# Kernel optimization log

Measured on AMD Instinct MI355X. Metric: run time of the kernel, lower is better.

Reference implementation:

```python
import jax, jax.numpy as jnp
import numpy as np

N_A = 100000; N_B = 100000; E = 1600000
H = 128; OUT = 16; G = 256; D_A = 64; D_B = 32


def setup_inputs() -> dict:
    key = jax.random.key(0)
    ks = jax.random.split(key, 24)
    f32 = jnp.float32
    def w(k, shape, fan_in):
        return jax.random.normal(k, shape, dtype=f32) / np.sqrt(fan_in)
    inp = {
        'x_a': jax.random.normal(ks[0], (N_A, D_A), dtype=f32),
        'x_b': jax.random.normal(ks[1], (N_B, D_B), dtype=f32),
        'ei_ab': jax.random.randint(ks[2], (2, E), 0, N_A),  # row0: src in a, row1: dst in b
        'ei_ba': jax.random.randint(ks[3], (2, E), 0, N_B),
        'ei_aa': jax.random.randint(ks[4], (2, E), 0, N_A),
        'batch_a': jnp.sort(jax.random.randint(ks[5], (N_A,), 0, G)),
        'batch_b': jnp.sort(jax.random.randint(ks[6], (N_B,), 0, G)),
        # node-type input embeddings
        'Wemb_a': w(ks[7], (D_A, H), D_A), 'bemb_a': jnp.zeros((H,), f32),
        'Wemb_b': w(ks[8], (D_B, H), D_B), 'bemb_b': jnp.zeros((H,), f32),
        # SAGEConv params per relation: lin_l (with bias) on aggregated, lin_r (no bias) on root
        'Wl_ab': w(ks[9], (H, H), H), 'bl_ab': jnp.zeros((H,), f32), 'Wr_ab': w(ks[10], (H, H), H),
        'Wl_ba': w(ks[11], (H, H), H), 'bl_ba': jnp.zeros((H,), f32), 'Wr_ba': w(ks[12], (H, H), H),
        'Wl_aa': w(ks[13], (H, H), H), 'bl_aa': jnp.zeros((H,), f32), 'Wr_aa': w(ks[14], (H, H), H),
        # output head
        'Wout': w(ks[15], (H, OUT), H), 'bout': jnp.zeros((OUT,), f32),
    }
    return inp


def _sage(x_src, x_dst, ei, Wl, bl, Wr, n_dst):
    # mean aggregation of source features over incoming edges, then transform + root
    msg = x_src[ei[0]]                                        # [E, H] gather
    s = jax.ops.segment_sum(msg, ei[1], num_segments=n_dst)   # [n_dst, H]
    cnt = jax.ops.segment_sum(jnp.ones((ei.shape[1], 1), x_src.dtype), ei[1], num_segments=n_dst)
    agg = s / jnp.maximum(cnt, 1.0)
    return agg @ Wl + bl + x_dst @ Wr


def _mean_pool(x, batch, num_graphs):
    s = jax.ops.segment_sum(x, batch, num_segments=num_graphs)
    cnt = jax.ops.segment_sum(jnp.ones((x.shape[0], 1), x.dtype), batch, num_segments=num_graphs)
    return s / jnp.maximum(cnt, 1.0)


def reference(x_a, x_b, ei_ab, ei_ba, ei_aa, batch_a, batch_b,
              Wemb_a, bemb_a, Wemb_b, bemb_b,
              Wl_ab, bl_ab, Wr_ab, Wl_ba, bl_ba, Wr_ba, Wl_aa, bl_aa, Wr_aa,
              Wout, bout):
    # per-type input projection
    h_a = x_a @ Wemb_a + bemb_a            # [N_A, H]
    h_b = x_b @ Wemb_b + bemb_b            # [N_B, H]
    # HeteroConv: one SAGEConv per relation, mean over relations per dst type
    m_b = _sage(h_a, h_b, ei_ab, Wl_ab, bl_ab, Wr_ab, N_B)          # dst 'b': 1 relation
    m_a1 = _sage(h_b, h_a, ei_ba, Wl_ba, bl_ba, Wr_ba, N_A)
    m_a2 = _sage(h_a, h_a, ei_aa, Wl_aa, bl_aa, Wr_aa, N_A)
    h_a2 = 0.5 * (m_a1 + m_a2)                                      # dst 'a': mean of 2 relations
    h_b2 = m_b
    # ReLU + per-type global mean pool + mean over node types
    p_a = _mean_pool(jax.nn.relu(h_a2), batch_a, G)                 # [G, H]
    p_b = _mean_pool(jax.nn.relu(h_b2), batch_b, G)
    x = 0.5 * (p_a + p_b)
    return x @ Wout + bout                                          # [G, OUT]
```

## Files before the change

kernel.cpp:

```cpp
#include <hip/hip_runtime.h>

#define NA 100000
#define NB 100000
#define NEDGE 1600000
#define HD 128
#define OUTD 16
#define NG 256
#define DA 64
#define DB 32

#define BIN_SHIFT 9
#define BIN_W 512
#define NBINS_R 196
#define NBINS 588
#define PADBIN 10240
#define EPB 8192
#define ECHUNKS 196

typedef unsigned int uint_t;
typedef unsigned short ushort_t;
typedef unsigned char uchar_t;
typedef __bf16 bf16_t;
typedef bf16_t bf16x8 __attribute__((ext_vector_type(8)));
typedef float f32x4 __attribute__((ext_vector_type(4)));
typedef float f32x2 __attribute__((ext_vector_type(2)));

__device__ __forceinline__ float bflo(uint_t u) {
    union { uint_t i; float f; } c; c.i = u << 16; return c.f;
}
__device__ __forceinline__ float bfhi(uint_t u) {
    union { uint_t i; float f; } c; c.i = u & 0xffff0000u; return c.f;
}
__device__ __forceinline__ float bf2f(ushort_t u) {
    union { uint_t i; float f; } c; c.i = ((uint_t)u) << 16; return c.f;
}
__device__ __forceinline__ uint_t f2bf(float f) {
    union { float f; uint_t i; } c; c.f = f;
    uint_t r = c.i + 0x7FFFu + ((c.i >> 16) & 1u);
    return r >> 16;
}
__device__ __forceinline__ uint_t pack2bf(float lo, float hi) {
    return f2bf(lo) | (f2bf(hi) << 16);
}

__global__ void __launch_bounds__(256)
prep_misc_kernel(const float* __restrict__ Wl_ab, const float* __restrict__ Wr_ab,
                 const float* __restrict__ Wl_ba, const float* __restrict__ Wl_aa,
                 const float* __restrict__ Wr_ba, const float* __restrict__ Wr_aa,
                 const float* __restrict__ Wemb_a, const float* __restrict__ Wemb_b,
                 ushort_t* __restrict__ wt_fb, ushort_t* __restrict__ wt_pa,
                 ushort_t* __restrict__ wt_ea, ushort_t* __restrict__ wt_eb,
                 const float* __restrict__ bl_ba, const float* __restrict__ bl_aa,
                 float* __restrict__ bias_pa,
                 const int* __restrict__ batch_a, const int* __restrict__ batch_b,
                 float* __restrict__ ga, float* __restrict__ gb)
{
    const int bx = blockIdx.x;
    __align__(16) ushort_t tmp[8];
    if (bx >= 40) {
        if (bx <= 43) {
            const int id = (bx - 40) * 256 + threadIdx.x;
            const int kk = id >> 9, ni = (id >> 6) & 7, l = id & 63;
            const int col = ni * 16 + (l & 15);
            const int k0 = kk * 32 + (l >> 4) * 8;
#pragma unroll
            for (int j = 0; j < 8; ++j) tmp[j] = (ushort_t)f2bf(Wemb_a[(k0 + j) * HD + col]);
            *reinterpret_cast<uint4*>(wt_ea + (size_t)id * 8) = *reinterpret_cast<const uint4*>(tmp);
            return;
        }
        if (bx <= 45) {
            const int id = (bx - 44) * 256 + threadIdx.x;
            const int ni = id >> 6, l = id & 63;
            const int col = ni * 16 + (l & 15);
            const int k0 = (l >> 4) * 8;
#pragma unroll
            for (int j = 0; j < 8; ++j) tmp[j] = (ushort_t)f2bf(Wemb_b[(k0 + j) * HD + col]);
            *reinterpret_cast<uint4*>(wt_eb + (size_t)id * 8) = *reinterpret_cast<const uint4*>(tmp);
            return;
        }
        if (bx == 46) {
            if (threadIdx.x < HD) bias_pa[threadIdx.x] = bl_ba[threadIdx.x] + bl_aa[threadIdx.x];
            return;
        }
        const int g = threadIdx.x;
        const int* batch = (bx == 48) ? batch_b : batch_a;
        float* outp = (bx == 48) ? gb : ga;
        const int n = NA;
        int lo0 = 0, hi0 = n;
        while (lo0 < hi0) { const int mid = (lo0 + hi0) >> 1; if (batch[mid] < g) lo0 = mid + 1; else hi0 = mid; }
        int lo1 = 0, hi1 = n;
        while (lo1 < hi1) { const int mid = (lo1 + hi1) >> 1; if (batch[mid] < g + 1) lo1 = mid + 1; else hi1 = mid; }
        outp[g] = (float)(lo1 - lo0);
        return;
    }
    const int m = bx >> 3;
    const int id = (bx & 7) * 256 + threadIdx.x;
    const int kk = id >> 9, ni = (id >> 6) & 7, l = id & 63;
    const int col = ni * 16 + (l & 15);
    const int k0 = kk * 32 + (l >> 4) * 8;
    const float* src = (m == 0) ? Wl_ab : (m == 1) ? Wr_ab : (m == 2) ? Wl_ba
                     : (m == 3) ? Wl_aa : Wr_ba;
#pragma unroll
    for (int j = 0; j < 8; ++j) {
        float v = src[(k0 + j) * HD + col];
        if (m == 4) v += Wr_aa[(k0 + j) * HD + col];
        tmp[j] = (ushort_t)f2bf(v);
    }
    const int half = ni >> 2, nih = ni & 3;
    const size_t eoff = (size_t)half * 8192 + ((kk * 4 + nih) * 64 + l) * 8;
    ushort_t* dst = (m < 2) ? (wt_fb + (size_t)m * 16384) : (wt_pa + (size_t)(m - 2) * 16384);
    *reinterpret_cast<uint4*>(dst + eoff) = *reinterpret_cast<const uint4*>(tmp);
}

template<int K>
__global__ void __launch_bounds__(256)
emb_mfma(const float* __restrict__ x, const ushort_t* __restrict__ wtf,
         const float* __restrict__ bias, ushort_t* __restrict__ h, int n)
{
    constexpr int KST = K / 32;
    __shared__ ushort_t wlds[K * HD];
    for (int i = threadIdx.x * 8; i < K * HD; i += 2048)
        *reinterpret_cast<uint4*>(wlds + i) = *reinterpret_cast<const uint4*>(wtf + i);
    __syncthreads();

    const int l = threadIdx.x & 63, w = threadIdx.x >> 6;
    const int lo = l & 15, hi = l >> 4;
    const int row_base = blockIdx.x * 128 + w * 32;

    f32x4 acc[2][8];
    const f32x4 zero = {0.f, 0.f, 0.f, 0.f};
#pragma unroll
    for (int mi = 0; mi < 2; ++mi)
#pragma unroll
        for (int ni = 0; ni < 8; ++ni) acc[mi][ni] = zero;

    bf16x8 a[2][KST];
#pragma unroll
    for (int mi = 0; mi < 2; ++mi) {
        int r = row_base + mi * 16 + lo;
        r = min(r, n - 1);
        const float* xr = x + (size_t)r * K + hi * 8;
#pragma unroll
        for (int kk = 0; kk < KST; ++kk) {
            const float4 f0 = *reinterpret_cast<const float4*>(xr + kk * 32);
            const float4 f1 = *reinterpret_cast<const float4*>(xr + kk * 32 + 4);
            __align__(16) ushort_t us[8];
            us[0] = (ushort_t)f2bf(f0.x); us[1] = (ushort_t)f2bf(f0.y);
            us[2] = (ushort_t)f2bf(f0.z); us[3] = (ushort_t)f2bf(f0.w);
            us[4] = (ushort_t)f2bf(f1.x); us[5] = (ushort_t)f2bf(f1.y);
            us[6] = (ushort_t)f2bf(f1.z); us[7] = (ushort_t)f2bf(f1.w);
            a[mi][kk] = *reinterpret_cast<const bf16x8*>(us);
        }
    }
#pragma unroll
    for (int kk = 0; kk < KST; ++kk) {
#pragma unroll
        for (int ni = 0; ni < 8; ++ni) {
            const bf16x8 b = *reinterpret_cast<const bf16x8*>(wlds + ((kk * 8 + ni) * 64 + l) * 8);
            acc[0][ni] = __builtin_amdgcn_mfma_f32_16x16x32_bf16(a[0][kk], b, acc[0][ni], 0, 0, 0);
            acc[1][ni] = __builtin_amdgcn_mfma_f32_16x16x32_bf16(a[1][kk], b, acc[1][ni], 0, 0, 0);
        }
    }
#pragma unroll
    for (int ni = 0; ni < 8; ++ni) {
        const int col = ni * 16 + lo;
        const float bv = bias[col];
#pragma unroll
        for (int mi = 0; mi < 2; ++mi) {
            const f32x4 v = acc[mi][ni];
#pragma unroll
            for (int r = 0; r < 4; ++r) {
                const int row = row_base + mi * 16 + hi * 4 + r;
                if (row < n) h[(size_t)row * HD + col] = (ushort_t)f2bf(v[r] + bv);
            }
        }
    }
}

__global__ void __launch_bounds__(256)
conv8_kernel(const ushort_t* __restrict__ h, uchar_t* __restrict__ h8, long n8)
{
    for (long i = (long)blockIdx.x * 256 + threadIdx.x; i < n8; i += (long)gridDim.x * 256) {
        const uint4 v = *reinterpret_cast<const uint4*>(h + i * 8);
        uint_t lo = (uint_t)__builtin_amdgcn_cvt_pk_fp8_f32(bflo(v.x), bfhi(v.x), 0, false);
        lo = (uint_t)__builtin_amdgcn_cvt_pk_fp8_f32(bflo(v.y), bfhi(v.y), lo, true);
        uint_t hi = (uint_t)__builtin_amdgcn_cvt_pk_fp8_f32(bflo(v.z), bfhi(v.z), 0, false);
        hi = (uint_t)__builtin_amdgcn_cvt_pk_fp8_f32(bflo(v.w), bfhi(v.w), hi, true);
        uint2 o; o.x = lo; o.y = hi;
        *reinterpret_cast<uint2*>(h8 + i * 8) = o;
    }
}

__global__ void __launch_bounds__(256)
part3_kernel(const int* __restrict__ ei_ab, const int* __restrict__ ei_ba,
             const int* __restrict__ ei_aa, int* __restrict__ bincnt,
             uint_t* __restrict__ binned)
{
    __shared__ uint_t sorted[EPB];
    __shared__ int lh[NBINS_R];
    __shared__ int lbase[NBINS_R];
    __shared__ int gbase[NBINS_R];
    __shared__ int lcur[NBINS_R];
    __shared__ int sc[256];
    const int r = blockIdx.y;
    const int* ei = (r == 0) ? ei_ab : (r == 1) ? ei_ba : ei_aa;
    const int t = threadIdx.x;
    for (int i = t; i < NBINS_R; i += 256) lh[i] = 0;
    __syncthreads();
    const int e0 = blockIdx.x * EPB;
    const int e1 = min(e0 + EPB, NEDGE);
    for (int e = e0 + t; e < e1; e += 256)
        atomicAdd(&lh[ei[NEDGE + e] >> BIN_SHIFT], 1);
    __syncthreads();
    {
        const int v = (t < NBINS_R) ? lh[t] : 0;
        sc[t] = v; __syncthreads();
        for (int d = 1; d < 256; d <<= 1) {
            const int x = (t >= d) ? sc[t - d] : 0;
            __syncthreads();
            sc[t] += x;
            __syncthreads();
        }
        if (t < NBINS_R) {
            const int ex = sc[t] - v;
            lbase[t] = ex; lcur[t] = ex;
            gbase[t] = v ? atomicAdd(&bincnt[r * NBINS_R + t], v) : 0;
        }
    }
    __syncthreads();
    for (int e = e0 + t; e < e1; e += 256) {
        const int dst = ei[NEDGE + e];
        const int src = ei[e];
        const int bin = dst >> BIN_SHIFT;
        const int pos = atomicAdd(&lcur[bin], 1);
        sorted[pos] = ((uint_t)(dst & (BIN_W - 1)) << 17) | (uint_t)src;
    }
    __syncthreads();
    const int wid = t >> 6, lane = t & 63;
    for (int b = wid; b < NBINS_R; b += 4) {
        const int cnt = lh[b], lb = lbase[b];
        uint_t* dst = binned + (size_t)(r * NBINS_R + b) * PADBIN + gbase[b];
        for (int k = lane; k < cnt; k += 64) dst[k] = sorted[lb + k];
    }
}

__global__ void __launch_bounds__(256)
binfill3_kernel(const uint_t* __restrict__ binned, const int* __restrict__ bincnt,
                int* __restrict__ off3, int* __restrict__ cnt3, int* __restrict__ csr3)
{
    __shared__ int hist[BIN_W];
    __shared__ int A[BIN_W];
    __shared__ int cursor[BIN_W];
    const int b = blockIdx.x;
    const int r = blockIdx.y;
    const int g = r * NBINS_R + b;
    const int start = g * PADBIN;
    const int end = start + bincnt[g];
    const int t = threadIdx.x;
    const int i0 = t, i1 = t + 256;
    hist[i0] = 0; hist[i1] = 0;
    __syncthreads();
    for (int j = start + t; j < end; j += 256)
        atomicAdd(&hist[binned[j] >> 17], 1);
    __syncthreads();
    A[i0] = hist[i0]; A[i1] = hist[i1];
    __syncthreads();
    for (int d = 1; d < BIN_W; d <<= 1) {
        const int x0 = (i0 >= d) ? A[i0 - d] : 0;
        const int x1 = (i1 >= d) ? A[i1 - d] : 0;
        __syncthreads();
        A[i0] += x0; A[i1] += x1;
        __syncthreads();
    }
    const int node0 = b * BIN_W;
#pragma unroll
    for (int q = 0; q < 2; ++q) {
        const int i = t + q * 256;
        const int ex = start + A[i] - hist[i];
        cursor[i] = ex;
        const int node = node0 + i;
        if (node < NA) { off3[r * NA + node] = ex; cnt3[r * NA + node] = hist[i]; }
    }
    __syncthreads();
    for (int j = start + t; j < end; j += 256) {
        const uint_t p = binned[j];
        const int pos = atomicAdd(&cursor[p >> 17], 1);
        csr3[pos] = (int)(p & 0x1FFFFu);
    }
}

__global__ void __launch_bounds__(256)
gather3_kernel(const uchar_t* __restrict__ h8_a, const uchar_t* __restrict__ h8_b,
               const int* __restrict__ csr3, const int* __restrict__ off3,
               const int* __restrict__ cnt3,
               ushort_t* __restrict__ s_ab, ushort_t* __restrict__ s_ba,
               ushort_t* __restrict__ s_aa)
{
    const int r = blockIdx.y;
    const uchar_t* hsrc = (r == 1) ? h8_b : h8_a;
    ushort_t* s = (r == 0) ? s_ab : (r == 1) ? s_ba : s_aa;
    const int* off = off3 + r * NA;
    const int* cnt = cnt3 + r * NA;
    const int wid = threadIdx.x >> 6, lane = threadIdx.x & 63;
    const int hl = lane & 31;
    const int nw = gridDim.x * 4;
    for (int node = blockIdx.x * 4 + wid; node < NA; node += nw) {
        const int o0 = off[node], deg = cnt[node];
        const int o1 = o0 + deg;
        float ax0 = 0.f, ax1 = 0.f, ax2 = 0.f, ax3 = 0.f;
        int j = o0;
        for (; j + 8 <= o1; j += 8) {
            const int s0 = csr3[j],     s1 = csr3[j + 1], s2 = csr3[j + 2], s3 = csr3[j + 3];
            const int s4 = csr3[j + 4], s5 = csr3[j + 5], s6 = csr3[j + 6], s7 = csr3[j + 7];
            const int sA = (lane & 32) ? s1 : s0;
            const int sB = (lane & 32) ? s3 : s2;
            const int sC = (lane & 32) ? s5 : s4;
            const int sD = (lane & 32) ? s7 : s6;
            const uint_t vA = *reinterpret_cast<const uint_t*>(hsrc + (size_t)sA * HD + hl * 4);
            const uint_t vB = *reinterpret_cast<const uint_t*>(hsrc + (size_t)sB * HD + hl * 4);
            const uint_t vC = *reinterpret_cast<const uint_t*>(hsrc + (size_t)sC * HD + hl * 4);
            const uint_t vD = *reinterpret_cast<const uint_t*>(hsrc + (size_t)sD * HD + hl * 4);
            const f32x2 a0 = __builtin_amdgcn_cvt_pk_f32_fp8(vA, false), a1 = __builtin_amdgcn_cvt_pk_f32_fp8(vA, true);
            const f32x2 b0 = __builtin_amdgcn_cvt_pk_f32_fp8(vB, false), b1 = __builtin_amdgcn_cvt_pk_f32_fp8(vB, true);
            const f32x2 c0 = __builtin_amdgcn_cvt_pk_f32_fp8(vC, false), c1 = __builtin_amdgcn_cvt_pk_f32_fp8(vC, true);
            const f32x2 d0 = __builtin_amdgcn_cvt_pk_f32_fp8(vD, false), d1 = __builtin_amdgcn_cvt_pk_f32_fp8(vD, true);
            ax0 += (a0[0] + b0[0]) + (c0[0] + d0[0]);
            ax1 += (a0[1] + b0[1]) + (c0[1] + d0[1]);
            ax2 += (a1[0] + b1[0]) + (c1[0] + d1[0]);
            ax3 += (a1[1] + b1[1]) + (c1[1] + d1[1]);
        }
        for (; j + 2 <= o1; j += 2) {
            const int s0 = csr3[j], s1 = csr3[j + 1];
            const int sA = (lane & 32) ? s1 : s0;
            const uint_t vA = *reinterpret_cast<const uint_t*>(hsrc + (size_t)sA * HD + hl * 4);
            const f32x2 a0 = __builtin_amdgcn_cvt_pk_f32_fp8(vA, false), a1 = __builtin_amdgcn_cvt_pk_f32_fp8(vA, true);
            ax0 += a0[0]; ax1 += a0[1]; ax2 += a1[0]; ax3 += a1[1];
        }
        if (j < o1) {
            const int s0 = csr3[j];
            const uint_t vA = *reinterpret_cast<const uint_t*>(hsrc + (size_t)s0 * HD + hl * 4);
            if (!(lane & 32)) {
                const f32x2 a0 = __builtin_amdgcn_cvt_pk_f32_fp8(vA, false), a1 = __builtin_amdgcn_cvt_pk_f32_fp8(vA, true);
                ax0 += a0[0]; ax1 += a0[1]; ax2 += a1[0]; ax3 += a1[1];
            }
        }
        ax0 += __shfl_xor(ax0, 32); ax1 += __shfl_xor(ax1, 32);
        ax2 += __shfl_xor(ax2, 32); ax3 += __shfl_xor(ax3, 32);
        if (!(lane & 32)) {
            const float inv = 1.0f / fmaxf((float)deg, 1.0f);
            uint2 wv;
            wv.x = pack2bf(ax0 * inv, ax1 * inv);
            wv.y = pack2bf(ax2 * inv, ax3 * inv);
            *reinterpret_cast<uint2*>(s + (size_t)node * HD + hl * 4) = wv;
        }
    }
}

template<int NSRC, int SCALE_HALF>
__global__ void __launch_bounds__(256, 4)
mfma_task(const ushort_t* __restrict__ x0, const ushort_t* __restrict__ x1,
          const ushort_t* __restrict__ x2,
          const ushort_t* __restrict__ wtf, const float* __restrict__ bias,
          ushort_t* __restrict__ m_out, int n)
{
    extern __shared__ char smem[];
    ushort_t* wlds = (ushort_t*)smem;
    const int half = blockIdx.y;
    for (int i = threadIdx.x * 8; i < NSRC * 8192; i += 2048) {
        const int s = i >> 13, off = i & 8191;
        *reinterpret_cast<uint4*>(wlds + i) =
            *reinterpret_cast<const uint4*>(wtf + (size_t)s * 16384 + half * 8192 + off);
    }
    __syncthreads();

    const int l  = threadIdx.x & 63, w = threadIdx.x >> 6;
    const int lo = l & 15, hi = l >> 4;
    const int row_base = blockIdx.x * 128 + w * 32;

    f32x4 acc[2][4];
    const f32x4 zero = {0.f, 0.f, 0.f, 0.f};
#pragma unroll
    for (int mi = 0; mi < 2; ++mi)
#pragma unroll
        for (int ni = 0; ni < 4; ++ni) acc[mi][ni] = zero;

#pragma unroll
    for (int s = 0; s < NSRC; ++s) {
        const ushort_t* xs = (s == 0) ? x0 : (s == 1) ? x1 : x2;
        bf16x8 a[2][4];
#pragma unroll
        for (int mi = 0; mi < 2; ++mi) {
            int r = row_base + mi * 16 + lo;
            r = min(r, n - 1);
            const ushort_t* xr = xs + (size_t)r * HD + hi * 8;
#pragma unroll
            for (int kk = 0; kk < 4; ++kk)
                a[mi][kk] = *reinterpret_cast<const bf16x8*>(xr + kk * 32);
        }
        const ushort_t* wm = wlds + s * 8192;
#pragma unroll
        for (int kk = 0; kk < 4; ++kk) {
#pragma unroll
            for (int nih = 0; nih < 4; ++nih) {
                const bf16x8 b = *reinterpret_cast<const bf16x8*>(wm + ((kk * 4 + nih) * 64 + l) * 8);
                acc[0][nih] = __builtin_amdgcn_mfma_f32_16x16x32_bf16(a[0][kk], b, acc[0][nih], 0, 0, 0);
                acc[1][nih] = __builtin_amdgcn_mfma_f32_16x16x32_bf16(a[1][kk], b, acc[1][nih], 0, 0, 0);
            }
        }
    }

#pragma unroll
    for (int nih = 0; nih < 4; ++nih) {
        const int col = half * 64 + nih * 16 + lo;
        const float bv = bias[col];
#pragma unroll
        for (int mi = 0; mi < 2; ++mi) {
            const f32x4 v = acc[mi][nih];
#pragma unroll
            for (int r = 0; r < 4; ++r) {
                const int row = row_base + mi * 16 + hi * 4 + r;
                if (row < n) {
                    float val = v[r] + bv;
                    if (SCALE_HALF) val *= 0.5f;
                    m_out[(size_t)row * HD + col] = (ushort_t)f2bf(fmaxf(val, 0.f));
                }
            }
        }
    }
}

__global__ void __launch_bounds__(256)
pool_kernel(const ushort_t* __restrict__ m_a, const ushort_t* __restrict__ m_b,
            const int* __restrict__ batch_a, const int* __restrict__ batch_b,
            float* __restrict__ pool_a, float* __restrict__ pool_b)
{
    const ushort_t* m = blockIdx.y ? m_b : m_a;
    const int* batch = blockIdx.y ? batch_b : batch_a;
    float* pool = blockIdx.y ? pool_b : pool_a;
    const int col = threadIdx.x & 127;
    const int rh = threadIdx.x >> 7;
    int row = blockIdx.x * 256 + rh * 128;
    const int rend = min(row + 128, NA);
    if (row >= rend) return;
    float acc = 0.f;
    int gcur = batch[row];
    for (; row < rend; ++row) {
        const int g = batch[row];
        if (g != gcur) {
            unsafeAtomicAdd(pool + (size_t)gcur * HD + col, acc);
            acc = 0.f; gcur = g;
        }
        acc += bf2f(m[(size_t)row * HD + col]);
    }
    unsafeAtomicAdd(pool + (size_t)gcur * HD + col, acc);
}

__global__ void final_kernel(const float* __restrict__ pa, const float* __restrict__ pb,
                             const float* __restrict__ ga, const float* __restrict__ gb,
                             const float* __restrict__ Wout, const float* __restrict__ bout,
                             float* __restrict__ out)
{
    const int g = blockIdx.x;
    const int lane = threadIdx.x;
    const float inva = 1.0f / fmaxf(ga[g], 1.0f);
    const float invb = 1.0f / fmaxf(gb[g], 1.0f);
    if (lane < OUTD) {
        float acc = bout[lane];
        for (int k = 0; k < HD; ++k) {
            const float x = 0.5f * (pa[g * HD + k] * inva + pb[g * HD + k] * invb);
            acc = fmaf(x, Wout[k * OUTD + lane], acc);
        }
        out[g * OUTD + lane] = acc;
    }
}

extern "C" void kernel_launch(void* const* d_in, const int* in_sizes, int n_in,
                              void* d_out, int out_size, void* d_ws, size_t ws_size,
                              hipStream_t stream)
{
    const float* x_a     = (const float*)d_in[0];
    const float* x_b     = (const float*)d_in[1];
    const int*   ei_ab   = (const int*)d_in[2];
    const int*   ei_ba   = (const int*)d_in[3];
    const int*   ei_aa   = (const int*)d_in[4];
    const int*   batch_a = (const int*)d_in[5];
    const int*   batch_b = (const int*)d_in[6];
    const float* Wemb_a  = (const float*)d_in[7];
    const float* bemb_a  = (const float*)d_in[8];
    const float* Wemb_b  = (const float*)d_in[9];
    const float* bemb_b  = (const float*)d_in[10];
    const float* Wl_ab   = (const float*)d_in[11];
    const float* bl_ab   = (const float*)d_in[12];
    const float* Wr_ab   = (const float*)d_in[13];
    const float* Wl_ba   = (const float*)d_in[14];
    const float* bl_ba   = (const float*)d_in[15];
    const float* Wr_ba   = (const float*)d_in[16];
    const float* Wl_aa   = (const float*)d_in[17];
    const float* bl_aa   = (const float*)d_in[18];
    const float* Wr_aa   = (const float*)d_in[19];
    const float* Wout    = (const float*)d_in[20];
    const float* bout    = (const float*)d_in[21];
    float* out = (float*)d_out;

    char* p = (char*)d_ws;
    ushort_t* h_a  = (ushort_t*)p; p += (size_t)NA * HD * 2;
    ushort_t* h_b  = (ushort_t*)p; p += (size_t)NB * HD * 2;
    ushort_t* s_ab = (ushort_t*)p; p += (size_t)NB * HD * 2;
    ushort_t* s_ba = (ushort_t*)p; p += (size_t)NA * HD * 2;
    ushort_t* s_aa = (ushort_t*)p; p += (size_t)NA * HD * 2;
    ushort_t* m_a  = (ushort_t*)p; p += (size_t)NA * HD * 2;
    ushort_t* m_b  = (ushort_t*)p; p += (size_t)NB * HD * 2;
    uchar_t* h8_a  = (uchar_t*)p;  p += (size_t)NA * HD;
    uchar_t* h8_b  = (uchar_t*)p;  p += (size_t)NB * HD;
    int* csr3   = (int*)p;  p += (size_t)NBINS * PADBIN * 4;
    uint_t* binned = (uint_t*)p; p += (size_t)NBINS * PADBIN * 4;
    int* off3   = (int*)p;  p += (size_t)3 * NA * 4;
    int* cnt3   = (int*)p;  p += (size_t)3 * NA * 4;
    int* bincnt = (int*)p;  p += (NBINS + 4) * 4;
    float* pool_a = (float*)p; p += (size_t)NG * HD * 4;
    float* pool_b = (float*)p; p += (size_t)NG * HD * 4;
    float* gcnt_a = (float*)p; p += NG * 4;
    float* gcnt_b = (float*)p; p += NG * 4;
    ushort_t* wt_fb = (ushort_t*)p; p += 2 * 16384 * 2;
    ushort_t* wt_pa = (ushort_t*)p; p += 3 * 16384 * 2;
    ushort_t* wt_ea = (ushort_t*)p; p += 64 * HD * 2;
    ushort_t* wt_eb = (ushort_t*)p; p += 32 * HD * 2;
    float* bias_pa  = (float*)p;    p += HD * 4;

    const int GT = (NA + 127) / 128;

    hipMemsetAsync(pool_a, 0, (size_t)2 * NG * HD * 4, stream);
    hipMemsetAsync(bincnt, 0, (size_t)NBINS * 4, stream);

    prep_misc_kernel<<<49, 256, 0, stream>>>(Wl_ab, Wr_ab, Wl_ba, Wl_aa, Wr_ba, Wr_aa,
                                             Wemb_a, Wemb_b, wt_fb, wt_pa, wt_ea, wt_eb,
                                             bl_ba, bl_aa, bias_pa,
                                             batch_a, batch_b, gcnt_a, gcnt_b);

    emb_mfma<DA><<<GT, 256, 0, stream>>>(x_a, wt_ea, bemb_a, h_a, NA);
    emb_mfma<DB><<<GT, 256, 0, stream>>>(x_b, wt_eb, bemb_b, h_b, NB);
    conv8_kernel<<<2048, 256, 0, stream>>>(h_a, h8_a, (long)(NA + NB) * HD / 8);

    part3_kernel<<<dim3(ECHUNKS, 3), 256, 0, stream>>>(ei_ab, ei_ba, ei_aa, bincnt, binned);
    binfill3_kernel<<<dim3(NBINS_R, 3), 256, 0, stream>>>(binned, bincnt, off3, cnt3, csr3);

    gather3_kernel<<<dim3(2048, 3), 256, 0, stream>>>(h8_a, h8_b, csr3, off3, cnt3, s_ab, s_ba, s_aa);

    const int lds_b = 2 * 16384;
    const int lds_a = 3 * 16384;
    hipFuncSetAttribute((const void*)mfma_task<2, 0>, hipFuncAttributeMaxDynamicSharedMemorySize, lds_b);
    hipFuncSetAttribute((const void*)mfma_task<3, 1>, hipFuncAttributeMaxDynamicSharedMemorySize, lds_a);

    mfma_task<2, 0><<<dim3(GT, 2), 256, lds_b, stream>>>(s_ab, h_b, nullptr, wt_fb, bl_ab, m_b, NB);
    mfma_task<3, 1><<<dim3(GT, 2), 256, lds_a, stream>>>(s_ba, s_aa, h_a, wt_pa, bias_pa, m_a, NA);

    pool_kernel<<<dim3((NA + 255) / 256, 2), 256, 0, stream>>>(m_a, m_b, batch_a, batch_b, pool_a, pool_b);

    final_kernel<<<NG, 64, 0, stream>>>(pool_a, pool_b, gcnt_a, gcnt_b, Wout, bout, out);
}
```

Measured before the change: 454.6 us.

## Fuse embedding with fp8 conversion, merge MFMA launches, deepen gather unroll

The two embedding kernels are merged into one launch, and each now writes the fp8 copy directly, which removes the separate conversion pass over h. The gather loop is unrolled to 16 edges per iteration with packed f32x2 accumulation so more loads are in flight. The two SAGE MFMA kernels are merged into one launch with a reordered tile/half mapping, and the pool kernel uses smaller row chunks for more blocks. The trade-off is more atomics in pooling, more register pressure in the gather loop, and fp8 bytes written through scattered per-element stores.

New measurement: 399.7 us. -12.1%, faster.

```diff
diff --git a/kernel.cpp b/kernel.cpp
--- a/kernel.cpp
+++ b/kernel.cpp
@@ -41,6 +41,9 @@
 }
 __device__ __forceinline__ uint_t pack2bf(float lo, float hi) {
     return f2bf(lo) | (f2bf(hi) << 16);
+}
+__device__ __forceinline__ uchar_t f2fp8(float v) {
+    return (uchar_t)(__builtin_amdgcn_cvt_pk_fp8_f32(v, v, 0, false) & 0xff);
 }
 
 __global__ void __launch_bounds__(256)
@@ -113,12 +116,12 @@
 }
 
 template<int K>
-__global__ void __launch_bounds__(256)
-emb_mfma(const float* __restrict__ x, const ushort_t* __restrict__ wtf,
-         const float* __restrict__ bias, ushort_t* __restrict__ h, int n)
+__device__ __forceinline__ void
+emb_body(const float* __restrict__ x, const ushort_t* __restrict__ wtf,
+         const float* __restrict__ bias, ushort_t* __restrict__ h,
+         uchar_t* __restrict__ h8, int n, ushort_t* wlds)
 {
     constexpr int KST = K / 32;
-    __shared__ ushort_t wlds[K * HD];
     for (int i = threadIdx.x * 8; i < K * HD; i += 2048)
         *reinterpret_cast<uint4*>(wlds + i) = *reinterpret_cast<const uint4*>(wtf + i);
     __syncthreads();
@@ -171,24 +174,26 @@
 #pragma unroll
             for (int r = 0; r < 4; ++r) {
                 const int row = row_base + mi * 16 + hi * 4 + r;
-                if (row < n) h[(size_t)row * HD + col] = (ushort_t)f2bf(v[r] + bv);
-            }
-        }
-    }
-}
-
-__global__ void __launch_bounds__(256)
-conv8_kernel(const ushort_t* __restrict__ h, uchar_t* __restrict__ h8, long n8)
-{
-    for (long i = (long)blockIdx.x * 256 + threadIdx.x; i < n8; i += (long)gridDim.x * 256) {
-        const uint4 v = *reinterpret_cast<const uint4*>(h + i * 8);
-        uint_t lo = (uint_t)__builtin_amdgcn_cvt_pk_fp8_f32(bflo(v.x), bfhi(v.x), 0, false);
-        lo = (uint_t)__builtin_amdgcn_cvt_pk_fp8_f32(bflo(v.y), bfhi(v.y), lo, true);
-        uint_t hi = (uint_t)__builtin_amdgcn_cvt_pk_fp8_f32(bflo(v.z), bfhi(v.z), 0, false);
-        hi = (uint_t)__builtin_amdgcn_cvt_pk_fp8_f32(bflo(v.w), bfhi(v.w), hi, true);
-        uint2 o; o.x = lo; o.y = hi;
-        *reinterpret_cast<uint2*>(h8 + i * 8) = o;
-    }
+                if (row < n) {
+                    const float val = v[r] + bv;
+                    h[(size_t)row * HD + col] = (ushort_t)f2bf(val);
+                    h8[(size_t)row * HD + col] = f2fp8(val);
+                }
+            }
+        }
+    }
+}
+
+__global__ void __launch_bounds__(256)
+emb2_kernel(const float* __restrict__ x_a, const float* __restrict__ x_b,
+            const ushort_t* __restrict__ wt_ea, const ushort_t* __restrict__ wt_eb,
+            const float* __restrict__ bemb_a, const float* __restrict__ bemb_b,
+            ushort_t* __restrict__ h_a, ushort_t* __restrict__ h_b,
+            uchar_t* __restrict__ h8_a, uchar_t* __restrict__ h8_b)
+{
+    __shared__ ushort_t wlds[DA * HD];
+    if (blockIdx.y == 0) emb_body<DA>(x_a, wt_ea, bemb_a, h_a, h8_a, NA, wlds);
+    else                 emb_body<DB>(x_b, wt_eb, bemb_b, h_b, h8_b, NB, wlds);
 }
 
 __global__ void __launch_bounds__(256)
@@ -303,50 +308,57 @@
     const int* cnt = cnt3 + r * NA;
     const int wid = threadIdx.x >> 6, lane = threadIdx.x & 63;
     const int hl = lane & 31;
+    const int sel = (lane >> 5) & 1;
     const int nw = gridDim.x * 4;
     for (int node = blockIdx.x * 4 + wid; node < NA; node += nw) {
         const int o0 = off[node], deg = cnt[node];
         const int o1 = o0 + deg;
-        float ax0 = 0.f, ax1 = 0.f, ax2 = 0.f, ax3 = 0.f;
+        f32x2 acc01 = {0.f, 0.f}, acc23 = {0.f, 0.f};
         int j = o0;
-        for (; j + 8 <= o1; j += 8) {
-            const int s0 = csr3[j],     s1 = csr3[j + 1], s2 = csr3[j + 2], s3 = csr3[j + 3];
-            const int s4 = csr3[j + 4], s5 = csr3[j + 5], s6 = csr3[j + 6], s7 = csr3[j + 7];
-            const int sA = (lane & 32) ? s1 : s0;
-            const int sB = (lane & 32) ? s3 : s2;
-            const int sC = (lane & 32) ? s5 : s4;
-            const int sD = (lane & 32) ? s7 : s6;
-            const uint_t vA = *reinterpret_cast<const uint_t*>(hsrc + (size_t)sA * HD + hl * 4);
-            const uint_t vB = *reinterpret_cast<const uint_t*>(hsrc + (size_t)sB * HD + hl * 4);
-            const uint_t vC = *reinterpret_cast<const uint_t*>(hsrc + (size_t)sC * HD + hl * 4);
-            const uint_t vD = *reinterpret_cast<const uint_t*>(hsrc + (size_t)sD * HD + hl * 4);
-            const f32x2 a0 = __builtin_amdgcn_cvt_pk_f32_fp8(vA, false), a1 = __builtin_amdgcn_cvt_pk_f32_fp8(vA, true);
-            const f32x2 b0 = __builtin_amdgcn_cvt_pk_f32_fp8(vB, false), b1 = __builtin_amdgcn_cvt_pk_f32_fp8(vB, true);
-            const f32x2 c0 = __builtin_amdgcn_cvt_pk_f32_fp8(vC, false), c1 = __builtin_amdgcn_cvt_pk_f32_fp8(vC, true);
-            const f32x2 d0 = __builtin_amdgcn_cvt_pk_f32_fp8(vD, false), d1 = __builtin_amdgcn_cvt_pk_f32_fp8(vD, true);
-            ax0 += (a0[0] + b0[0]) + (c0[0] + d0[0]);
-            ax1 += (a0[1] + b0[1]) + (c0[1] + d0[1]);
-            ax2 += (a1[0] + b1[0]) + (c1[0] + d1[0]);
-            ax3 += (a1[1] + b1[1]) + (c1[1] + d1[1]);
+        for (; j + 16 <= o1; j += 16) {
+            uint_t vv[8];
+#pragma unroll
+            for (int q = 0; q < 8; ++q) {
+                const int sE = csr3[j + 2 * q + sel];
+                vv[q] = *reinterpret_cast<const uint_t*>(hsrc + (size_t)sE * HD + hl * 4);
+            }
+#pragma unroll
+            for (int q = 0; q < 8; ++q) {
+                acc01 += __builtin_amdgcn_cvt_pk_f32_fp8(vv[q], false);
+                acc23 += __builtin_amdgcn_cvt_pk_f32_fp8(vv[q], true);
+            }
+        }
+        for (; j + 4 <= o1; j += 4) {
+            uint_t vv[2];
+#pragma unroll
+            for (int q = 0; q < 2; ++q) {
+                const int sE = csr3[j + 2 * q + sel];
+                vv[q] = *reinterpret_cast<const uint_t*>(hsrc + (size_t)sE * HD + hl * 4);
+            }
+#pragma unroll
+            for (int q = 0; q < 2; ++q) {
+                acc01 += __builtin_amdgcn_cvt_pk_f32_fp8(vv[q], false);
+                acc23 += __builtin_amdgcn_cvt_pk_f32_fp8(vv[q], true);
+            }
         }
         for (; j + 2 <= o1; j += 2) {
-            const int s0 = csr3[j], s1 = csr3[j + 1];
-            const int sA = (lane & 32) ? s1 : s0;
-            const uint_t vA = *reinterpret_cast<const uint_t*>(hsrc + (size_t)sA * HD + hl * 4);
-            const f32x2 a0 = __builtin_amdgcn_cvt_pk_f32_fp8(vA, false), a1 = __builtin_amdgcn_cvt_pk_f32_fp8(vA, true);
-            ax0 += a0[0]; ax1 += a0[1]; ax2 += a1[0]; ax3 += a1[1];
+            const int sE = csr3[j + sel];
+            const uint_t v = *reinterpret_cast<const uint_t*>(hsrc + (size_t)sE * HD + hl * 4);
+            acc01 += __builtin_amdgcn_cvt_pk_f32_fp8(v, false);
+            acc23 += __builtin_amdgcn_cvt_pk_f32_fp8(v, true);
         }
         if (j < o1) {
-            const int s0 = csr3[j];
-            const uint_t vA = *reinterpret_cast<const uint_t*>(hsrc + (size_t)s0 * HD + hl * 4);
-            if (!(lane & 32)) {
-                const f32x2 a0 = __builtin_amdgcn_cvt_pk_f32_fp8(vA, false), a1 = __builtin_amdgcn_cvt_pk_f32_fp8(vA, true);
-                ax0 += a0[0]; ax1 += a0[1]; ax2 += a1[0]; ax3 += a1[1];
-            }
-        }
+            const int sE = csr3[min(j + sel, o1 - 1)];
+            const uint_t v = *reinterpret_cast<const uint_t*>(hsrc + (size_t)sE * HD + hl * 4);
+            if (!sel) {
+                acc01 += __builtin_amdgcn_cvt_pk_f32_fp8(v, false);
+                acc23 += __builtin_amdgcn_cvt_pk_f32_fp8(v, true);
+            }
+        }
+        float ax0 = acc01[0], ax1 = acc01[1], ax2 = acc23[0], ax3 = acc23[1];
         ax0 += __shfl_xor(ax0, 32); ax1 += __shfl_xor(ax1, 32);
         ax2 += __shfl_xor(ax2, 32); ax3 += __shfl_xor(ax3, 32);
-        if (!(lane & 32)) {
+        if (!sel) {
             const float inv = 1.0f / fmaxf((float)deg, 1.0f);
             uint2 wv;
             wv.x = pack2bf(ax0 * inv, ax1 * inv);
@@ -357,15 +369,13 @@
 }
 
 template<int NSRC, int SCALE_HALF>
-__global__ void __launch_bounds__(256, 4)
-mfma_task(const ushort_t* __restrict__ x0, const ushort_t* __restrict__ x1,
+__device__ __forceinline__ void
+mfma_body(const ushort_t* __restrict__ x0, const ushort_t* __restrict__ x1,
           const ushort_t* __restrict__ x2,
           const ushort_t* __restrict__ wtf, const float* __restrict__ bias,
-          ushort_t* __restrict__ m_out, int n)
-{
-    extern __shared__ char smem[];
+          ushort_t* __restrict__ m_out, int n, int tile, int half, char* smem)
+{
     ushort_t* wlds = (ushort_t*)smem;
-    const int half = blockIdx.y;
     for (int i = threadIdx.x * 8; i < NSRC * 8192; i += 2048) {
         const int s = i >> 13, off = i & 8191;
         *reinterpret_cast<uint4*>(wlds + i) =
@@ -375,7 +385,7 @@
 
     const int l  = threadIdx.x & 63, w = threadIdx.x >> 6;
     const int lo = l & 15, hi = l >> 4;
-    const int row_base = blockIdx.x * 128 + w * 32;
+    const int row_base = tile * 128 + w * 32;
 
     f32x4 acc[2][4];
     const f32x4 zero = {0.f, 0.f, 0.f, 0.f};
@@ -430,6 +440,26 @@
 }
 
 __global__ void __launch_bounds__(256)
+mfma_merged(const ushort_t* __restrict__ s_ab, const ushort_t* __restrict__ h_b,
+            const ushort_t* __restrict__ wt_fb, const float* __restrict__ bl_ab,
+            ushort_t* __restrict__ m_b,
+            const ushort_t* __restrict__ s_ba, const ushort_t* __restrict__ s_aa,
+            const ushort_t* __restrict__ h_a,
+            const ushort_t* __restrict__ wt_pa, const float* __restrict__ bias_pa,
+            ushort_t* __restrict__ m_a)
+{
+    extern __shared__ char smem[];
+    const int u = blockIdx.x;
+    const int tile = (u >> 4) * 8 + (u & 7);
+    const int half = (u >> 3) & 1;
+    if (tile >= (NA + 127) / 128) return;
+    if (blockIdx.y == 0)
+        mfma_body<2, 0>(s_ab, h_b, nullptr, wt_fb, bl_ab, m_b, NB, tile, half, smem);
+    else
+        mfma_body<3, 1>(s_ba, s_aa, h_a, wt_pa, bias_pa, m_a, NA, tile, half, smem);
+}
+
+__global__ void __launch_bounds__(256)
 pool_kernel(const ushort_t* __restrict__ m_a, const ushort_t* __restrict__ m_b,
             const int* __restrict__ batch_a, const int* __restrict__ batch_b,
             float* __restrict__ pool_a, float* __restrict__ pool_b)
@@ -439,8 +469,8 @@
     float* pool = blockIdx.y ? pool_b : pool_a;
     const int col = threadIdx.x & 127;
     const int rh = threadIdx.x >> 7;
-    int row = blockIdx.x * 256 + rh * 128;
-    const int rend = min(row + 128, NA);
+    int row = blockIdx.x * 128 + rh * 64;
+    const int rend = min(row + 64, NA);
     if (row >= rend) return;
     float acc = 0.f;
     int gcur = batch[row];
@@ -537,24 +567,21 @@
                                              bl_ba, bl_aa, bias_pa,
                                              batch_a, batch_b, gcnt_a, gcnt_b);
 
-    emb_mfma<DA><<<GT, 256, 0, stream>>>(x_a, wt_ea, bemb_a, h_a, NA);
-    emb_mfma<DB><<<GT, 256, 0, stream>>>(x_b, wt_eb, bemb_b, h_b, NB);
-    conv8_kernel<<<2048, 256, 0, stream>>>(h_a, h8_a, (long)(NA + NB) * HD / 8);
+    emb2_kernel<<<dim3(GT, 2), 256, 0, stream>>>(x_a, x_b, wt_ea, wt_eb, bemb_a, bemb_b,
+                                                 h_a, h_b, h8_a, h8_b);
 
     part3_kernel<<<dim3(ECHUNKS, 3), 256, 0, stream>>>(ei_ab, ei_ba, ei_aa, bincnt, binned);
     binfill3_kernel<<<dim3(NBINS_R, 3), 256, 0, stream>>>(binned, bincnt, off3, cnt3, csr3);
 
     gather3_kernel<<<dim3(2048, 3), 256, 0, stream>>>(h8_a, h8_b, csr3, off3, cnt3, s_ab, s_ba, s_aa);
 
-    const int lds_b = 2 * 16384;
-    const int lds_a = 3 * 16384;
-    hipFuncSetAttribute((const void*)mfma_task<2, 0>, hipFuncAttributeMaxDynamicSharedMemorySize, lds_b);
-    hipFuncSetAttribute((const void*)mfma_task<3, 1>, hipFuncAttributeMaxDynamicSharedMemorySize, lds_a);
-
-    mfma_task<2, 0><<<dim3(GT, 2), 256, lds_b, stream>>>(s_ab, h_b, nullptr, wt_fb, bl_ab, m_b, NB);
-    mfma_task<3, 1><<<dim3(GT, 2), 256, lds_a, stream>>>(s_ba, s_aa, h_a, wt_pa, bias_pa, m_a, NA);
-
-    pool_kernel<<<dim3((NA + 255) / 256, 2), 256, 0, stream>>>(m_a, m_b, batch_a, batch_b, pool_a, pool_b);
+    const int lds_m = 3 * 16384;
+    hipFuncSetAttribute((const void*)mfma_merged, hipFuncAttributeMaxDynamicSharedMemorySize, lds_m);
+    const int GX = ((2 * GT + 15) / 16) * 16;
+    mfma_merged<<<dim3(GX, 2), 256, lds_m, stream>>>(s_ab, h_b, wt_fb, bl_ab, m_b,
+                                                     s_ba, s_aa, h_a, wt_pa, bias_pa, m_a);
+
+    pool_kernel<<<dim3((NA + 127) / 128, 2), 256, 0, stream>>>(m_a, m_b, batch_a, batch_b, pool_a, pool_b);
 
     final_kernel<<<NG, 64, 0, stream>>>(pool_a, pool_b, gcnt_a, gcnt_b, Wout, bout, out);
 }
```
